# Optimization experiments

Measured on AMD Instinct MI355X. Metric: run time of the kernel, lower is better.

The kernel has to match this reference:

```python
import jax, jax.numpy as jnp
import numpy as np

B, T, HID = 4, 2048, 1024
NH = 16
HS = HID // NH  # 64


def setup_inputs() -> dict:
    key = jax.random.key(0)
    ks = jax.random.split(key, 9)
    s = 1.0 / np.sqrt(HID)
    return {
        "x": jax.random.normal(ks[0], (B, T, HID), dtype=jnp.float32),
        "Wq": jax.random.uniform(ks[1], (HID, HID), jnp.float32, -s, s),
        "bq": jax.random.uniform(ks[2], (HID,), jnp.float32, -s, s),
        "Wk": jax.random.uniform(ks[3], (HID, HID), jnp.float32, -s, s),
        "bk": jax.random.uniform(ks[4], (HID,), jnp.float32, -s, s),
        "Wv": jax.random.uniform(ks[5], (HID, HS), jnp.float32, -s, s),
        "bv": jax.random.uniform(ks[6], (HS,), jnp.float32, -s, s),
        "Wo": jax.random.uniform(ks[7], (HS, HID), jnp.float32, -1.0 / np.sqrt(HS), 1.0 / np.sqrt(HS)),
        "bo": jax.random.uniform(ks[8], (HID,), jnp.float32, -1.0 / np.sqrt(HS), 1.0 / np.sqrt(HS)),
    }


def reference(x, Wq, bq, Wk, bk, Wv, bv, Wo, bo):
    scale = HS ** -0.5
    q = (x @ Wq + bq).reshape(B, T, NH, HS)  # (B,T,H,hs)
    k = (x @ Wk + bk).reshape(B, T, NH, HS)
    v = x @ Wv + bv                          # shared V: (B,T,hs)
    # scores: (B,H,T,T)
    scores = jnp.einsum("bqhd,bkhd->bhqk", q, k) * scale
    attn = jax.nn.softmax(scores, axis=-1)
    attn_avg = attn.mean(axis=1)             # (B,T,T), head-averaged
    out = jnp.einsum("bqk,bkd->bqd", attn_avg, v) @ Wo + bo  # (B,T,HID)
    return out, attn_avg
```

## Files before the change

### kernel.cpp

```cpp
#include <hip/hip_runtime.h>
#include <math.h>

#define Bc   4
#define Tt   2048
#define HIDc 1024
#define NHc  16
#define HSc  64
#define BTc  (Bc * Tt)
#define QSCALE 0.18033688011112042f

typedef __attribute__((ext_vector_type(8))) short bf16x8;
typedef __attribute__((ext_vector_type(4))) float f32x4;

__device__ __forceinline__ unsigned short f2bf(float f) {
    unsigned u = __float_as_uint(f);
    u = u + 0x7FFFu + ((u >> 16) & 1u);
    return (unsigned short)(u >> 16);
}

__device__ __forceinline__ float fexp2(float x) {
#if __has_builtin(__builtin_amdgcn_exp2f)
    return __builtin_amdgcn_exp2f(x);
#else
    float r; asm("v_exp_f32 %0, %1" : "=v"(r) : "v"(x)); return r;
#endif
}

__global__ __launch_bounds__(256) void gemm_f32(
    const float* __restrict__ A, const float* __restrict__ Bm,
    const float* __restrict__ bias, float* __restrict__ C,
    int M, int N, int K, long sA, long sB, long sC)
{
    A  += (long)blockIdx.z * sA;
    Bm += (long)blockIdx.z * sB;
    C  += (long)blockIdx.z * sC;

    __shared__ float As[16][64];
    __shared__ float Bs[16][64];

    const int tid  = threadIdx.x;
    const int tx   = tid & 15;
    const int ty   = tid >> 4;
    const int row0 = blockIdx.y * 64;
    const int col0 = blockIdx.x * 64;

    const int la_r = tid >> 2;
    const int la_c = (tid & 3) << 2;
    const int lb_r = tid >> 4;
    const int lb_c = (tid & 15) << 2;

    float acc[4][4] = {};

    for (int k0 = 0; k0 < K; k0 += 16) {
        float4 av = *(const float4*)&A[(long)(row0 + la_r) * K + k0 + la_c];
        float4 bv = *(const float4*)&Bm[(long)(k0 + lb_r) * N + col0 + lb_c];
        __syncthreads();
        As[la_c + 0][la_r] = av.x;
        As[la_c + 1][la_r] = av.y;
        As[la_c + 2][la_r] = av.z;
        As[la_c + 3][la_r] = av.w;
        *(float4*)&Bs[lb_r][lb_c] = bv;
        __syncthreads();
#pragma unroll
        for (int kk = 0; kk < 16; ++kk) {
            float4 a = *(float4*)&As[kk][ty << 2];
            float4 b = *(float4*)&Bs[kk][tx << 2];
            float ar[4] = {a.x, a.y, a.z, a.w};
            float br[4] = {b.x, b.y, b.z, b.w};
#pragma unroll
            for (int i = 0; i < 4; ++i)
#pragma unroll
                for (int j = 0; j < 4; ++j)
                    acc[i][j] = fmaf(ar[i], br[j], acc[i][j]);
        }
    }

    float4 bvv = make_float4(0.f, 0.f, 0.f, 0.f);
    if (bias) bvv = *(const float4*)&bias[col0 + (tx << 2)];
#pragma unroll
    for (int i = 0; i < 4; ++i) {
        int m = row0 + (ty << 2) + i;
        float4 o;
        o.x = acc[i][0] + bvv.x;
        o.y = acc[i][1] + bvv.y;
        o.z = acc[i][2] + bvv.z;
        o.w = acc[i][3] + bvv.w;
        *(float4*)&C[(long)m * N + col0 + (tx << 2)] = o;
    }
}

__global__ __launch_bounds__(256) void init_bias64(
    float* __restrict__ C, const float* __restrict__ bias, long n)
{
    long idx = (long)blockIdx.x * 256 + threadIdx.x;
    if (idx < n) C[idx] = bias ? bias[idx & 63] : 0.f;
}

__global__ __launch_bounds__(256) void cast_bf16(
    const float* __restrict__ src, unsigned short* __restrict__ dst, long n)
{
    long i = ((long)blockIdx.x * 256 + threadIdx.x) * 4;
    if (i >= n) return;
    float4 v = *(const float4*)&src[i];
    ushort4 o;
    o.x = f2bf(v.x); o.y = f2bf(v.y); o.z = f2bf(v.z); o.w = f2bf(v.w);
    *(ushort4*)&dst[i] = o;
}

__global__ __launch_bounds__(256) void transpose_cast(
    const float* __restrict__ W, unsigned short* __restrict__ Wt, int R, int C)
{
    __shared__ float t[32][33];
    const int k0 = blockIdx.x * 32, n0 = blockIdx.y * 32;
    const int c = threadIdx.x & 31, r = threadIdx.x >> 5;
#pragma unroll
    for (int rr = r; rr < 32; rr += 8)
        t[rr][c] = W[(long)(k0 + rr) * C + n0 + c];
    __syncthreads();
#pragma unroll
    for (int rr = r; rr < 32; rr += 8)
        Wt[(long)(n0 + rr) * R + k0 + c] = f2bf(t[c][rr]);
}

__global__ __launch_bounds__(256) void gemm_bt_bf16(
    const unsigned short* __restrict__ A, const unsigned short* __restrict__ Bt,
    const float* __restrict__ bias, unsigned short* __restrict__ C,
    int M, int N, int K, float oscale)
{
    __shared__ unsigned short As[128][72];
    __shared__ unsigned short Bs[128][72];

    const int tid  = threadIdx.x;
    const int row0 = blockIdx.y * 128;
    const int col0 = blockIdx.x * 128;
    const int w  = tid >> 6, L = tid & 63;
    const int wm = (w & 1) * 64, wn = (w >> 1) * 64;
    const int lr = tid >> 3;
    const int lc = (tid & 7) * 8;
    const int ml = L & 15, q8 = (L >> 4) * 8, q4 = (L >> 4) * 4;

    f32x4 acc[4][4];
#pragma unroll
    for (int i = 0; i < 4; ++i)
#pragma unroll
        for (int j = 0; j < 4; ++j)
            acc[i][j] = (f32x4){0.f, 0.f, 0.f, 0.f};

    for (int k0 = 0; k0 < K; k0 += 64) {
        __syncthreads();
#pragma unroll
        for (int rr = 0; rr < 128; rr += 32) {
            *(float4*)&As[lr + rr][lc] = *(const float4*)&A[(long)(row0 + lr + rr) * K + k0 + lc];
            *(float4*)&Bs[lr + rr][lc] = *(const float4*)&Bt[(long)(col0 + lr + rr) * K + k0 + lc];
        }
        __syncthreads();
#pragma unroll
        for (int kk = 0; kk < 64; kk += 32) {
            bf16x8 a[4], b[4];
#pragma unroll
            for (int i = 0; i < 4; ++i) a[i] = *(bf16x8*)&As[wm + i * 16 + ml][kk + q8];
#pragma unroll
            for (int j = 0; j < 4; ++j) b[j] = *(bf16x8*)&Bs[wn + j * 16 + ml][kk + q8];
#pragma unroll
            for (int i = 0; i < 4; ++i)
#pragma unroll
                for (int j = 0; j < 4; ++j)
                    acc[i][j] = __builtin_amdgcn_mfma_f32_16x16x32_bf16(a[i], b[j], acc[i][j], 0, 0, 0);
        }
    }

#pragma unroll
    for (int j = 0; j < 4; ++j) {
        const int col = col0 + wn + j * 16 + ml;
        const float bj = bias ? bias[col] : 0.f;
#pragma unroll
        for (int i = 0; i < 4; ++i) {
#pragma unroll
            for (int r = 0; r < 4; ++r) {
                const int row = row0 + wm + i * 16 + q4 + r;
                C[(long)row * N + col] = f2bf((acc[i][j][r] + bj) * oscale);
            }
        }
    }
}

__global__ __launch_bounds__(256) void gemm_v_bf16(
    const unsigned short* __restrict__ A, const unsigned short* __restrict__ Bt,
    float* __restrict__ C)
{
    __shared__ unsigned short As[128][72];
    __shared__ unsigned short Bs[64][72];

    const int tid  = threadIdx.x;
    const int row0 = blockIdx.x * 128;
    const int kbeg = blockIdx.y * 256;
    const int w = tid >> 6, L = tid & 63;
    const int ml = L & 15, q8 = (L >> 4) * 8, q4 = (L >> 4) * 4;
    const int ar = tid >> 3, ac = (tid & 7) * 8;
    const int br = tid >> 2, bc = (tid & 3) * 16;

    f32x4 acc[2][4];
#pragma unroll
    for (int i = 0; i < 2; ++i)
#pragma unroll
        for (int j = 0; j < 4; ++j) acc[i][j] = (f32x4){0.f, 0.f, 0.f, 0.f};

    for (int k0 = kbeg; k0 < kbeg + 256; k0 += 64) {
        __syncthreads();
#pragma unroll
        for (int rr = 0; rr < 128; rr += 32)
            *(float4*)&As[ar + rr][ac] = *(const float4*)&A[(long)(row0 + ar + rr) * HIDc + k0 + ac];
        *(float4*)&Bs[br][bc]     = *(const float4*)&Bt[(long)br * HIDc + k0 + bc];
        *(float4*)&Bs[br][bc + 8] = *(const float4*)&Bt[(long)br * HIDc + k0 + bc + 8];
        __syncthreads();
#pragma unroll
        for (int kk = 0; kk < 64; kk += 32) {
            bf16x8 a[2], b[4];
#pragma unroll
            for (int i = 0; i < 2; ++i) a[i] = *(bf16x8*)&As[w * 32 + i * 16 + ml][kk + q8];
#pragma unroll
            for (int j = 0; j < 4; ++j) b[j] = *(bf16x8*)&Bs[j * 16 + ml][kk + q8];
#pragma unroll
            for (int i = 0; i < 2; ++i)
#pragma unroll
                for (int j = 0; j < 4; ++j)
                    acc[i][j] = __builtin_amdgcn_mfma_f32_16x16x32_bf16(a[i], b[j], acc[i][j], 0, 0, 0);
        }
    }

#pragma unroll
    for (int i = 0; i < 2; ++i)
#pragma unroll
        for (int j = 0; j < 4; ++j)
#pragma unroll
            for (int r = 0; r < 4; ++r)
                atomicAdd(&C[(long)(row0 + w * 32 + i * 16 + q4 + r) * 64 + j * 16 + ml], acc[i][j][r]);
}

__global__ __launch_bounds__(256) void attn_denom(
    const unsigned short* __restrict__ qb, const unsigned short* __restrict__ kb,
    float* __restrict__ linv)
{
    const int qt = blockIdx.x, h = blockIdx.y, b = blockIdx.z;
    __shared__ unsigned short Qs[128][72];
    __shared__ unsigned short Ks[64][72];

    const int tid = threadIdx.x;
    const int w = tid >> 6, L = tid & 63;
    const int ml = L & 15, q8 = (L >> 4) * 8, q4 = (L >> 4) * 4;
    const int ar = tid >> 3, ac = (tid & 7) * 8;
    const int kr = tid >> 2, kc = (tid & 3) * 16;

#pragma unroll
    for (int rr = 0; rr < 128; rr += 32)
        *(float4*)&Qs[ar + rr][ac] =
            *(const float4*)&qb[(long)(b * Tt + qt * 128 + ar + rr) * HIDc + h * HSc + ac];

    float lacc[2][4] = {};

    for (int kt = 0; kt < Tt / 64; ++kt) {
        const unsigned short* s = kb + ((long)(b * Tt + kt * 64 + kr) * HIDc + h * HSc + kc);
        float4 v0 = *(const float4*)s;
        float4 v1 = *(const float4*)(s + 8);
        __syncthreads();
        *(float4*)&Ks[kr][kc]     = v0;
        *(float4*)&Ks[kr][kc + 8] = v1;
        __syncthreads();

        f32x4 acc[2][4];
#pragma unroll
        for (int i = 0; i < 2; ++i)
#pragma unroll
            for (int j = 0; j < 4; ++j) acc[i][j] = (f32x4){0.f, 0.f, 0.f, 0.f};
#pragma unroll
        for (int kk = 0; kk < 64; kk += 32) {
            bf16x8 a[2], bfr[4];
#pragma unroll
            for (int i = 0; i < 2; ++i) a[i] = *(bf16x8*)&Qs[w * 32 + i * 16 + ml][kk + q8];
#pragma unroll
            for (int j = 0; j < 4; ++j) bfr[j] = *(bf16x8*)&Ks[j * 16 + ml][kk + q8];
#pragma unroll
            for (int i = 0; i < 2; ++i)
#pragma unroll
                for (int j = 0; j < 4; ++j)
                    acc[i][j] = __builtin_amdgcn_mfma_f32_16x16x32_bf16(a[i], bfr[j], acc[i][j], 0, 0, 0);
        }
#pragma unroll
        for (int i = 0; i < 2; ++i)
#pragma unroll
            for (int j = 0; j < 4; ++j)
#pragma unroll
                for (int r = 0; r < 4; ++r)
                    lacc[i][r] += fexp2(acc[i][j][r]);
    }

#pragma unroll
    for (int i = 0; i < 2; ++i)
#pragma unroll
        for (int r = 0; r < 4; ++r) {
            float v = lacc[i][r];
            v += __shfl_xor(v, 1, 16);
            v += __shfl_xor(v, 2, 16);
            v += __shfl_xor(v, 4, 16);
            v += __shfl_xor(v, 8, 16);
            if (ml == 0)
                linv[((long)(b * NHc + h)) * Tt + qt * 128 + w * 32 + i * 16 + q4 + r] =
                    1.0f / (v * (float)NHc);
        }
}

__global__ __launch_bounds__(256) void attn_avg_w(
    const unsigned short* __restrict__ qb, const unsigned short* __restrict__ kb,
    const float* __restrict__ linv, const float* __restrict__ v,
    float* __restrict__ attn, float* __restrict__ o1)
{
    const int ktg = blockIdx.x, qt = blockIdx.y, b = blockIdx.z;

    __shared__ __align__(16) unsigned char smem[34816];
    unsigned short (*Qs)[72]   = (unsigned short(*)[72])smem;
    unsigned short (*Ks)[72]   = (unsigned short(*)[72])(smem + 9216);
    float* invs                = (float*)(smem + 27648);
    unsigned short (*Ps)[136]  = (unsigned short(*)[136])smem;
    unsigned short (*Vst)[136] = (unsigned short(*)[136])(smem + 17408);

    const int tid = threadIdx.x;
    const int w = tid >> 6, L = tid & 63;
    const int ml = L & 15, q8 = (L >> 4) * 8, q4 = (L >> 4) * 4;
    const int rw = (w >> 1) * 32;
    const int kh = (w & 1) * 64;
    const int qr = tid >> 2, qc = (tid & 3) * 16;
    const int kr = tid >> 3, kc = (tid & 7) * 8;

    float pacc[2][4][4] = {};

    for (int h = 0; h < NHc; ++h) {
        const unsigned short* sq = qb + ((long)(b * Tt + qt * 64 + qr) * HIDc + h * HSc + qc);
        float4 q0 = *(const float4*)sq;
        float4 q1 = *(const float4*)(sq + 8);
        float4 kv[4];
#pragma unroll
        for (int rr = 0; rr < 4; ++rr)
            kv[rr] = *(const float4*)&kb[(long)(b * Tt + ktg * 128 + kr + rr * 32) * HIDc + h * HSc + kc];
        float iv = 0.f;
        if (tid < 64) iv = linv[((long)(b * NHc + h)) * Tt + qt * 64 + tid];
        __syncthreads();
        *(float4*)&Qs[qr][qc]     = q0;
        *(float4*)&Qs[qr][qc + 8] = q1;
#pragma unroll
        for (int rr = 0; rr < 4; ++rr)
            *(float4*)&Ks[kr + rr * 32][kc] = kv[rr];
        if (tid < 64) invs[tid] = iv;
        __syncthreads();

        f32x4 acc[2][4];
#pragma unroll
        for (int i = 0; i < 2; ++i)
#pragma unroll
            for (int j = 0; j < 4; ++j) acc[i][j] = (f32x4){0.f, 0.f, 0.f, 0.f};
#pragma unroll
        for (int kk = 0; kk < 64; kk += 32) {
            bf16x8 a[2], bfr[4];
#pragma unroll
            for (int i = 0; i < 2; ++i) a[i] = *(bf16x8*)&Qs[rw + i * 16 + ml][kk + q8];
#pragma unroll
            for (int j = 0; j < 4; ++j) bfr[j] = *(bf16x8*)&Ks[kh + j * 16 + ml][kk + q8];
#pragma unroll
            for (int i = 0; i < 2; ++i)
#pragma unroll
                for (int j = 0; j < 4; ++j)
                    acc[i][j] = __builtin_amdgcn_mfma_f32_16x16x32_bf16(a[i], bfr[j], acc[i][j], 0, 0, 0);
        }
        float ivr[2][4];
#pragma unroll
        for (int i = 0; i < 2; ++i)
#pragma unroll
            for (int r = 0; r < 4; ++r) ivr[i][r] = invs[rw + i * 16 + q4 + r];
#pragma unroll
        for (int i = 0; i < 2; ++i)
#pragma unroll
            for (int j = 0; j < 4; ++j)
#pragma unroll
                for (int r = 0; r < 4; ++r)
                    pacc[i][j][r] += fexp2(acc[i][j][r]) * ivr[i][r];
    }

    __syncthreads();

#pragma unroll
    for (int i = 0; i < 2; ++i)
#pragma unroll
        for (int j = 0; j < 4; ++j)
#pragma unroll
            for (int r = 0; r < 4; ++r) {
                const int qrow = rw + i * 16 + q4 + r;
                const int col  = kh + j * 16 + ml;
                attn[((long)(b * Tt + qt * 64 + qrow)) * Tt + ktg * 128 + col] = pacc[i][j][r];
                Ps[qrow][col] = f2bf(pacc[i][j][r]);
            }
#pragma unroll
    for (int e = tid; e < 8192; e += 256) {
        const int r = e >> 6, d = e & 63;
        Vst[d][r] = f2bf(v[((long)(b * Tt + ktg * 128 + r)) * 64 + d]);
    }
    __syncthreads();

    const int qh = (w >> 1) * 32, dh = (w & 1) * 32;
    f32x4 uacc[2][2];
#pragma unroll
    for (int i = 0; i < 2; ++i)
#pragma unroll
        for (int j = 0; j < 2; ++j) uacc[i][j] = (f32x4){0.f, 0.f, 0.f, 0.f};
#pragma unroll
    for (int kk = 0; kk < 128; kk += 32) {
        bf16x8 a0 = *(bf16x8*)&Ps[qh + ml][kk + q8];
        bf16x8 a1 = *(bf16x8*)&Ps[qh + 16 + ml][kk + q8];
        bf16x8 b0 = *(bf16x8*)&Vst[dh + ml][kk + q8];
        bf16x8 b1 = *(bf16x8*)&Vst[dh + 16 + ml][kk + q8];
        uacc[0][0] = __builtin_amdgcn_mfma_f32_16x16x32_bf16(a0, b0, uacc[0][0], 0, 0, 0);
        uacc[0][1] = __builtin_amdgcn_mfma_f32_16x16x32_bf16(a0, b1, uacc[0][1], 0, 0, 0);
        uacc[1][0] = __builtin_amdgcn_mfma_f32_16x16x32_bf16(a1, b0, uacc[1][0], 0, 0, 0);
        uacc[1][1] = __builtin_amdgcn_mfma_f32_16x16x32_bf16(a1, b1, uacc[1][1], 0, 0, 0);
    }
#pragma unroll
    for (int i = 0; i < 2; ++i)
#pragma unroll
        for (int j = 0; j < 2; ++j)
#pragma unroll
            for (int r = 0; r < 4; ++r)
                atomicAdd(&o1[((long)(b * Tt + qt * 64 + qh + i * 16 + q4 + r)) * 64 + dh + j * 16 + ml],
                          uacc[i][j][r]);
}

extern "C" void kernel_launch(void* const* d_in, const int* in_sizes, int n_in,
                              void* d_out, int out_size, void* d_ws, size_t ws_size,
                              hipStream_t stream)
{
    const float* x  = (const float*)d_in[0];
    const float* Wq = (const float*)d_in[1];
    const float* bq = (const float*)d_in[2];
    const float* Wk = (const float*)d_in[3];
    const float* bk = (const float*)d_in[4];
    const float* Wv = (const float*)d_in[5];
    const float* bv = (const float*)d_in[6];
    const float* Wo = (const float*)d_in[7];
    const float* bo = (const float*)d_in[8];

    float* out  = (float*)d_out;
    float* attn = out + (long)BTc * HIDc;

    unsigned short* xb  = (unsigned short*)d_ws;
    unsigned short* Wqt = xb  + (long)BTc * HIDc;
    unsigned short* Wkt = Wqt + (long)HIDc * HIDc;
    unsigned short* Wvt = Wkt + (long)HIDc * HIDc;
    unsigned short* qb  = Wvt + (long)HSc * HIDc;
    unsigned short* kb  = qb  + (long)BTc * HIDc;
    float* v    = (float*)(kb + (long)BTc * HIDc);
    float* linv = v    + (long)BTc * HSc;
    float* o1   = linv + (long)Bc * NHc * Tt;

    dim3 blk(256);

    cast_bf16<<<dim3((BTc * HIDc) / 1024), blk, 0, stream>>>(x, xb, (long)BTc * HIDc);
    transpose_cast<<<dim3(32, 32), blk, 0, stream>>>(Wq, Wqt, HIDc, HIDc);
    transpose_cast<<<dim3(32, 32), blk, 0, stream>>>(Wk, Wkt, HIDc, HIDc);
    transpose_cast<<<dim3(32, 2),  blk, 0, stream>>>(Wv, Wvt, HIDc, HSc);
    init_bias64<<<dim3((BTc * HSc) / 256), blk, 0, stream>>>(v,  bv,      (long)BTc * HSc);
    init_bias64<<<dim3((BTc * HSc) / 256), blk, 0, stream>>>(o1, nullptr, (long)BTc * HSc);

    gemm_bt_bf16<<<dim3(HIDc / 128, BTc / 128), blk, 0, stream>>>(xb, Wqt, bq, qb, BTc, HIDc, HIDc, QSCALE);
    gemm_bt_bf16<<<dim3(HIDc / 128, BTc / 128), blk, 0, stream>>>(xb, Wkt, bk, kb, BTc, HIDc, HIDc, 1.0f);

    gemm_v_bf16<<<dim3(BTc / 128, HIDc / 256), blk, 0, stream>>>(xb, Wvt, v);

    attn_denom<<<dim3(Tt / 128, NHc, Bc), blk, 0, stream>>>(qb, kb, linv);

    attn_avg_w<<<dim3(Tt / 128, Tt / 64, Bc), blk, 0, stream>>>(qb, kb, linv, v, attn, o1);

    gemm_f32<<<dim3(HIDc / 64, BTc / 64, 1), blk, 0, stream>>>(o1, Wo, bo, out, BTc, HIDc, HSc, 0, 0, 0);
}
```

Measured before the change: 446.3 us.

## Split PV product into separate GEMM, prefetch Q/K tiles, drop atomics

Removes the fused P·V step and its atomicAdds from attn_avg_w. The head-averaged attention is instead written to the output and read back by a new gemm_pv kernel, which splits the key dimension in half into two partial buffers that are summed when gemm_f32 loads its A operand. V is transposed and cast to bf16 up front by reusing the weight workspaces. attn_denom and attn_avg_w now register-prefetch the next K/Q tile during the current one, and all per-head inverse denominators are loaded into shared memory once. The cost is re-reading the large fp32 attention matrix from memory, in exchange for avoiding atomic contention and gaining better overlap.

```diff
diff --git a/kernel.cpp b/kernel.cpp
--- a/kernel.cpp
+++ b/kernel.cpp
@@ -27,14 +27,10 @@
 }
 
 __global__ __launch_bounds__(256) void gemm_f32(
-    const float* __restrict__ A, const float* __restrict__ Bm,
-    const float* __restrict__ bias, float* __restrict__ C,
-    int M, int N, int K, long sA, long sB, long sC)
-{
-    A  += (long)blockIdx.z * sA;
-    Bm += (long)blockIdx.z * sB;
-    C  += (long)blockIdx.z * sC;
-
+    const float* __restrict__ A, const float* __restrict__ A2,
+    const float* __restrict__ Bm, const float* __restrict__ bias,
+    float* __restrict__ C, int M, int N, int K)
+{
     __shared__ float As[16][64];
     __shared__ float Bs[16][64];
 
@@ -53,6 +49,10 @@
 
     for (int k0 = 0; k0 < K; k0 += 16) {
         float4 av = *(const float4*)&A[(long)(row0 + la_r) * K + k0 + la_c];
+        if (A2) {
+            float4 a2 = *(const float4*)&A2[(long)(row0 + la_r) * K + k0 + la_c];
+            av.x += a2.x; av.y += a2.y; av.z += a2.z; av.w += a2.w;
+        }
         float4 bv = *(const float4*)&Bm[(long)(k0 + lb_r) * N + col0 + lb_c];
         __syncthreads();
         As[la_c + 0][la_r] = av.x;
@@ -256,15 +256,20 @@
         *(float4*)&Qs[ar + rr][ac] =
             *(const float4*)&qb[(long)(b * Tt + qt * 128 + ar + rr) * HIDc + h * HSc + ac];
 
+    const unsigned short* kbase = kb + ((long)(b * Tt + kr) * HIDc + h * HSc + kc);
+    float4 v0 = *(const float4*)kbase;
+    float4 v1 = *(const float4*)(kbase + 8);
+
     float lacc[2][4] = {};
 
     for (int kt = 0; kt < Tt / 64; ++kt) {
-        const unsigned short* s = kb + ((long)(b * Tt + kt * 64 + kr) * HIDc + h * HSc + kc);
-        float4 v0 = *(const float4*)s;
-        float4 v1 = *(const float4*)(s + 8);
-        __syncthreads();
         *(float4*)&Ks[kr][kc]     = v0;
         *(float4*)&Ks[kr][kc + 8] = v1;
+        if (kt + 1 < Tt / 64) {
+            const unsigned short* s = kbase + (long)(kt + 1) * 64 * HIDc;
+            v0 = *(const float4*)s;
+            v1 = *(const float4*)(s + 8);
+        }
         __syncthreads();
 
         f32x4 acc[2][4];
@@ -292,6 +297,7 @@
 #pragma unroll
                 for (int r = 0; r < 4; ++r)
                     lacc[i][r] += fexp2(acc[i][j][r]);
+        __syncthreads();
     }
 
 #pragma unroll
@@ -311,17 +317,13 @@
 
 __global__ __launch_bounds__(256) void attn_avg_w(
     const unsigned short* __restrict__ qb, const unsigned short* __restrict__ kb,
-    const float* __restrict__ linv, const float* __restrict__ v,
-    float* __restrict__ attn, float* __restrict__ o1)
+    const float* __restrict__ linv, float* __restrict__ attn)
 {
     const int ktg = blockIdx.x, qt = blockIdx.y, b = blockIdx.z;
 
-    __shared__ __align__(16) unsigned char smem[34816];
-    unsigned short (*Qs)[72]   = (unsigned short(*)[72])smem;
-    unsigned short (*Ks)[72]   = (unsigned short(*)[72])(smem + 9216);
-    float* invs                = (float*)(smem + 27648);
-    unsigned short (*Ps)[136]  = (unsigned short(*)[136])smem;
-    unsigned short (*Vst)[136] = (unsigned short(*)[136])(smem + 17408);
+    __shared__ unsigned short Qs[64][72];
+    __shared__ unsigned short Ks[128][72];
+    __shared__ float invsAll[NHc][64];
 
     const int tid = threadIdx.x;
     const int w = tid >> 6, L = tid & 63;
@@ -331,25 +333,39 @@
     const int qr = tid >> 2, qc = (tid & 3) * 16;
     const int kr = tid >> 3, kc = (tid & 7) * 8;
 
+    {
+        const int hh = tid >> 4, r4 = (tid & 15) * 4;
+        *(float4*)&invsAll[hh][r4] =
+            *(const float4*)&linv[((long)(b * NHc + hh)) * Tt + qt * 64 + r4];
+    }
+
+    const unsigned short* qbase = qb + ((long)(b * Tt + qt * 64 + qr) * HIDc + qc);
+    const unsigned short* kbase = kb + ((long)(b * Tt + ktg * 128 + kr) * HIDc + kc);
+
+    float4 q0 = *(const float4*)qbase;
+    float4 q1 = *(const float4*)(qbase + 8);
+    float4 kv[4];
+#pragma unroll
+    for (int rr = 0; rr < 4; ++rr)
+        kv[rr] = *(const float4*)(kbase + (long)rr * 32 * HIDc);
+
     float pacc[2][4][4] = {};
 
     for (int h = 0; h < NHc; ++h) {
-        const unsigned short* sq = qb + ((long)(b * Tt + qt * 64 + qr) * HIDc + h * HSc + qc);
-        float4 q0 = *(const float4*)sq;
-        float4 q1 = *(const float4*)(sq + 8);
-        float4 kv[4];
-#pragma unroll
-        for (int rr = 0; rr < 4; ++rr)
-            kv[rr] = *(const float4*)&kb[(long)(b * Tt + ktg * 128 + kr + rr * 32) * HIDc + h * HSc + kc];
-        float iv = 0.f;
-        if (tid < 64) iv = linv[((long)(b * NHc + h)) * Tt + qt * 64 + tid];
-        __syncthreads();
         *(float4*)&Qs[qr][qc]     = q0;
         *(float4*)&Qs[qr][qc + 8] = q1;
 #pragma unroll
         for (int rr = 0; rr < 4; ++rr)
             *(float4*)&Ks[kr + rr * 32][kc] = kv[rr];
-        if (tid < 64) invs[tid] = iv;
+        if (h + 1 < NHc) {
+            const unsigned short* sq = qbase + (h + 1) * HSc;
+            q0 = *(const float4*)sq;
+            q1 = *(const float4*)(sq + 8);
+            const unsigned short* sk = kbase + (h + 1) * HSc;
+#pragma unroll
+            for (int rr = 0; rr < 4; ++rr)
+                kv[rr] = *(const float4*)(sk + (long)rr * 32 * HIDc);
+        }
         __syncthreads();
 
         f32x4 acc[2][4];
@@ -371,10 +387,8 @@
                     acc[i][j] = __builtin_amdgcn_mfma_f32_16x16x32_bf16(a[i], bfr[j], acc[i][j], 0, 0, 0);
         }
         float ivr[2][4];
-#pragma unroll
-        for (int i = 0; i < 2; ++i)
-#pragma unroll
-            for (int r = 0; r < 4; ++r) ivr[i][r] = invs[rw + i * 16 + q4 + r];
+        *(float4*)&ivr[0][0] = *(const float4*)&invsAll[h][rw + q4];
+        *(float4*)&ivr[1][0] = *(const float4*)&invsAll[h][rw + 16 + q4];
 #pragma unroll
         for (int i = 0; i < 2; ++i)
 #pragma unroll
@@ -382,9 +396,8 @@
 #pragma unroll
                 for (int r = 0; r < 4; ++r)
                     pacc[i][j][r] += fexp2(acc[i][j][r]) * ivr[i][r];
-    }
-
-    __syncthreads();
+        __syncthreads();
+    }
 
 #pragma unroll
     for (int i = 0; i < 2; ++i)
@@ -395,40 +408,84 @@
                 const int qrow = rw + i * 16 + q4 + r;
                 const int col  = kh + j * 16 + ml;
                 attn[((long)(b * Tt + qt * 64 + qrow)) * Tt + ktg * 128 + col] = pacc[i][j][r];
-                Ps[qrow][col] = f2bf(pacc[i][j][r]);
             }
-#pragma unroll
-    for (int e = tid; e < 8192; e += 256) {
-        const int r = e >> 6, d = e & 63;
-        Vst[d][r] = f2bf(v[((long)(b * Tt + ktg * 128 + r)) * 64 + d]);
-    }
-    __syncthreads();
-
-    const int qh = (w >> 1) * 32, dh = (w & 1) * 32;
-    f32x4 uacc[2][2];
+}
+
+__global__ __launch_bounds__(256) void gemm_pv(
+    const float* __restrict__ attn, const unsigned short* __restrict__ vT,
+    float* __restrict__ o1a, float* __restrict__ o1b)
+{
+    const int qt = blockIdx.x, khalf = blockIdx.y, b = blockIdx.z;
+    float* o1p = khalf ? o1b : o1a;
+
+    __shared__ unsigned short Ps[64][72];
+    __shared__ unsigned short Vs[64][72];
+
+    const int tid = threadIdx.x;
+    const int w = tid >> 6, L = tid & 63;
+    const int ml = L & 15, q8 = (L >> 4) * 8, q4 = (L >> 4) * 4;
+    const int wq = (w >> 1) * 32, wd = (w & 1) * 32;
+    const int pr = tid >> 2, pc = (tid & 3) * 16;
+    const int vr = tid >> 3, vc = (tid & 7) * 8;
+
+    const float* abase = attn + ((long)(b * Tt + qt * 64 + pr)) * Tt + khalf * 1024 + pc;
+    const unsigned short* vbase = vT + ((long)(b * HSc + vr)) * Tt + khalf * 1024 + vc;
+
+    float4 pf[4], vf0, vf1;
+#pragma unroll
+    for (int i = 0; i < 4; ++i) pf[i] = *(const float4*)(abase + i * 4);
+    vf0 = *(const float4*)vbase;
+    vf1 = *(const float4*)(vbase + (long)32 * Tt);
+
+    f32x4 acc[2][2];
 #pragma unroll
     for (int i = 0; i < 2; ++i)
 #pragma unroll
-        for (int j = 0; j < 2; ++j) uacc[i][j] = (f32x4){0.f, 0.f, 0.f, 0.f};
-#pragma unroll
-    for (int kk = 0; kk < 128; kk += 32) {
-        bf16x8 a0 = *(bf16x8*)&Ps[qh + ml][kk + q8];
-        bf16x8 a1 = *(bf16x8*)&Ps[qh + 16 + ml][kk + q8];
-        bf16x8 b0 = *(bf16x8*)&Vst[dh + ml][kk + q8];
-        bf16x8 b1 = *(bf16x8*)&Vst[dh + 16 + ml][kk + q8];
-        uacc[0][0] = __builtin_amdgcn_mfma_f32_16x16x32_bf16(a0, b0, uacc[0][0], 0, 0, 0);
-        uacc[0][1] = __builtin_amdgcn_mfma_f32_16x16x32_bf16(a0, b1, uacc[0][1], 0, 0, 0);
-        uacc[1][0] = __builtin_amdgcn_mfma_f32_16x16x32_bf16(a1, b0, uacc[1][0], 0, 0, 0);
-        uacc[1][1] = __builtin_amdgcn_mfma_f32_16x16x32_bf16(a1, b1, uacc[1][1], 0, 0, 0);
-    }
+        for (int j = 0; j < 2; ++j) acc[i][j] = (f32x4){0.f, 0.f, 0.f, 0.f};
+
+    for (int t = 0; t < 16; ++t) {
+        __align__(16) unsigned short tmp[16];
+#pragma unroll
+        for (int i = 0; i < 4; ++i) {
+            tmp[i * 4 + 0] = f2bf(pf[i].x);
+            tmp[i * 4 + 1] = f2bf(pf[i].y);
+            tmp[i * 4 + 2] = f2bf(pf[i].z);
+            tmp[i * 4 + 3] = f2bf(pf[i].w);
+        }
+        *(float4*)&Ps[pr][pc]      = *(float4*)&tmp[0];
+        *(float4*)&Ps[pr][pc + 8]  = *(float4*)&tmp[8];
+        *(float4*)&Vs[vr][vc]      = vf0;
+        *(float4*)&Vs[vr + 32][vc] = vf1;
+        if (t + 1 < 16) {
+#pragma unroll
+            for (int i = 0; i < 4; ++i)
+                pf[i] = *(const float4*)(abase + (t + 1) * 64 + i * 4);
+            vf0 = *(const float4*)(vbase + (t + 1) * 64);
+            vf1 = *(const float4*)(vbase + (long)32 * Tt + (t + 1) * 64);
+        }
+        __syncthreads();
+#pragma unroll
+        for (int kk = 0; kk < 64; kk += 32) {
+            bf16x8 a0 = *(bf16x8*)&Ps[wq + ml][kk + q8];
+            bf16x8 a1 = *(bf16x8*)&Ps[wq + 16 + ml][kk + q8];
+            bf16x8 b0 = *(bf16x8*)&Vs[wd + ml][kk + q8];
+            bf16x8 b1 = *(bf16x8*)&Vs[wd + 16 + ml][kk + q8];
+            acc[0][0] = __builtin_amdgcn_mfma_f32_16x16x32_bf16(a0, b0, acc[0][0], 0, 0, 0);
+            acc[0][1] = __builtin_amdgcn_mfma_f32_16x16x32_bf16(a0, b1, acc[0][1], 0, 0, 0);
+            acc[1][0] = __builtin_amdgcn_mfma_f32_16x16x32_bf16(a1, b0, acc[1][0], 0, 0, 0);
+            acc[1][1] = __builtin_amdgcn_mfma_f32_16x16x32_bf16(a1, b1, acc[1][1], 0, 0, 0);
+        }
+        __syncthreads();
+    }
+
 #pragma unroll
     for (int i = 0; i < 2; ++i)
 #pragma unroll
         for (int j = 0; j < 2; ++j)
 #pragma unroll
             for (int r = 0; r < 4; ++r)
-                atomicAdd(&o1[((long)(b * Tt + qt * 64 + qh + i * 16 + q4 + r)) * 64 + dh + j * 16 + ml],
-                          uacc[i][j][r]);
+                o1p[((long)(b * Tt + qt * 64 + wq + i * 16 + q4 + r)) * HSc + wd + j * 16 + ml] =
+                    acc[i][j][r];
 }
 
 extern "C" void kernel_launch(void* const* d_in, const int* in_sizes, int n_in,
@@ -456,7 +513,9 @@
     unsigned short* kb  = qb  + (long)BTc * HIDc;
     float* v    = (float*)(kb + (long)BTc * HIDc);
     float* linv = v    + (long)BTc * HSc;
-    float* o1   = linv + (long)Bc * NHc * Tt;
+    float* o1a  = linv + (long)Bc * NHc * Tt;
+    unsigned short* vbT = Wqt;
+    float* o1b = (float*)Wkt;
 
     dim3 blk(256);
 
@@ -464,17 +523,22 @@
     transpose_cast<<<dim3(32, 32), blk, 0, stream>>>(Wq, Wqt, HIDc, HIDc);
     transpose_cast<<<dim3(32, 32), blk, 0, stream>>>(Wk, Wkt, HIDc, HIDc);
     transpose_cast<<<dim3(32, 2),  blk, 0, stream>>>(Wv, Wvt, HIDc, HSc);
-    init_bias64<<<dim3((BTc * HSc) / 256), blk, 0, stream>>>(v,  bv,      (long)BTc * HSc);
-    init_bias64<<<dim3((BTc * HSc) / 256), blk, 0, stream>>>(o1, nullptr, (long)BTc * HSc);
+    init_bias64<<<dim3((BTc * HSc) / 256), blk, 0, stream>>>(v, bv, (long)BTc * HSc);
 
     gemm_bt_bf16<<<dim3(HIDc / 128, BTc / 128), blk, 0, stream>>>(xb, Wqt, bq, qb, BTc, HIDc, HIDc, QSCALE);
     gemm_bt_bf16<<<dim3(HIDc / 128, BTc / 128), blk, 0, stream>>>(xb, Wkt, bk, kb, BTc, HIDc, HIDc, 1.0f);
 
     gemm_v_bf16<<<dim3(BTc / 128, HIDc / 256), blk, 0, stream>>>(xb, Wvt, v);
 
+    for (int bi = 0; bi < Bc; ++bi)
+        transpose_cast<<<dim3(Tt / 32, HSc / 32), blk, 0, stream>>>(
+            v + (long)bi * Tt * HSc, vbT + (long)bi * HSc * Tt, Tt, HSc);
+
     attn_denom<<<dim3(Tt / 128, NHc, Bc), blk, 0, stream>>>(qb, kb, linv);
 
-    attn_avg_w<<<dim3(Tt / 128, Tt / 64, Bc), blk, 0, stream>>>(qb, kb, linv, v, attn, o1);
-
-    gemm_f32<<<dim3(HIDc / 64, BTc / 64, 1), blk, 0, stream>>>(o1, Wo, bo, out, BTc, HIDc, HSc, 0, 0, 0);
-}
+    attn_avg_w<<<dim3(Tt / 128, Tt / 64, Bc), blk, 0, stream>>>(qb, kb, linv, attn);
+
+    gemm_pv<<<dim3(Tt / 64, 2, Bc), blk, 0, stream>>>(attn, vbT, o1a, o1b);
+
+    gemm_f32<<<dim3(HIDc / 64, BTc / 64), blk, 0, stream>>>(o1a, o1b, Wo, bo, out, BTc, HIDc, HSc);
+}
```

Result: slower. 466.6 us (+4.6%).

## Remap blocks for XCD locality, enlarge attention tile, prefetch Q/K tiles

Applied to the files above, without the earlier changes.

Blocks of the GEMMs, denominator and attention-average kernels are now launched on a 1D grid and remapped so that consecutive blocks on the same XCD share rows and batches, which aims to improve L2 reuse on MI355X's chiplets. The attention-average kernel grows its query tile from 64 to 128 rows per block, halving the grid and the redundant K loads per query. It also preloads all head inverse-denominators into shared memory and register-prefetches the next head's Q/K. The denominator kernel gets the same register prefetch. The cost is more registers and shared memory per block (52 KB), which can reduce occupancy.

```diff
diff --git a/kernel.cpp b/kernel.cpp
--- a/kernel.cpp
+++ b/kernel.cpp
@@ -29,12 +29,8 @@
 __global__ __launch_bounds__(256) void gemm_f32(
     const float* __restrict__ A, const float* __restrict__ Bm,
     const float* __restrict__ bias, float* __restrict__ C,
-    int M, int N, int K, long sA, long sB, long sC)
-{
-    A  += (long)blockIdx.z * sA;
-    Bm += (long)blockIdx.z * sB;
-    C  += (long)blockIdx.z * sC;
-
+    int M, int N, int K)
+{
     __shared__ float As[16][64];
     __shared__ float Bs[16][64];
 
@@ -130,9 +126,12 @@
     __shared__ unsigned short As[128][72];
     __shared__ unsigned short Bs[128][72];
 
+    const int gid = blockIdx.x;
+    const int xcd = gid & 7, ii = gid >> 3;
+    const int row0 = (xcd * 8 + (ii >> 3)) * 128;
+    const int col0 = (ii & 7) * 128;
+
     const int tid  = threadIdx.x;
-    const int row0 = blockIdx.y * 128;
-    const int col0 = blockIdx.x * 128;
     const int w  = tid >> 6, L = tid & 63;
     const int wm = (w & 1) * 64, wn = (w >> 1) * 64;
     const int lr = tid >> 3;
@@ -191,9 +190,12 @@
     __shared__ unsigned short As[128][72];
     __shared__ unsigned short Bs[64][72];
 
+    const int gid = blockIdx.x;
+    const int xcd = gid & 7, ii = gid >> 3;
+    const int row0 = (xcd * 8 + (ii >> 2)) * 128;
+    const int kbeg = (ii & 3) * 256;
+
     const int tid  = threadIdx.x;
-    const int row0 = blockIdx.x * 128;
-    const int kbeg = blockIdx.y * 256;
     const int w = tid >> 6, L = tid & 63;
     const int ml = L & 15, q8 = (L >> 4) * 8, q4 = (L >> 4) * 4;
     const int ar = tid >> 3, ac = (tid & 7) * 8;
@@ -241,7 +243,12 @@
     const unsigned short* __restrict__ qb, const unsigned short* __restrict__ kb,
     float* __restrict__ linv)
 {
-    const int qt = blockIdx.x, h = blockIdx.y, b = blockIdx.z;
+    const int gid = blockIdx.x;
+    const int xcd = gid & 7, ii = gid >> 3;
+    const int bh  = xcd * 8 + (ii >> 4);
+    const int qt  = ii & 15;
+    const int b   = bh >> 4, h = bh & 15;
+
     __shared__ unsigned short Qs[128][72];
     __shared__ unsigned short Ks[64][72];
 
@@ -256,15 +263,20 @@
         *(float4*)&Qs[ar + rr][ac] =
             *(const float4*)&qb[(long)(b * Tt + qt * 128 + ar + rr) * HIDc + h * HSc + ac];
 
+    const unsigned short* kbase = kb + ((long)(b * Tt + kr) * HIDc + h * HSc + kc);
+    float4 v0 = *(const float4*)kbase;
+    float4 v1 = *(const float4*)(kbase + 8);
+
     float lacc[2][4] = {};
 
     for (int kt = 0; kt < Tt / 64; ++kt) {
-        const unsigned short* s = kb + ((long)(b * Tt + kt * 64 + kr) * HIDc + h * HSc + kc);
-        float4 v0 = *(const float4*)s;
-        float4 v1 = *(const float4*)(s + 8);
-        __syncthreads();
         *(float4*)&Ks[kr][kc]     = v0;
         *(float4*)&Ks[kr][kc + 8] = v1;
+        if (kt + 1 < Tt / 64) {
+            const unsigned short* s = kbase + (long)(kt + 1) * 64 * HIDc;
+            v0 = *(const float4*)s;
+            v1 = *(const float4*)(s + 8);
+        }
         __syncthreads();
 
         f32x4 acc[2][4];
@@ -292,6 +304,7 @@
 #pragma unroll
                 for (int r = 0; r < 4; ++r)
                     lacc[i][r] += fexp2(acc[i][j][r]);
+        __syncthreads();
     }
 
 #pragma unroll
@@ -314,87 +327,105 @@
     const float* __restrict__ linv, const float* __restrict__ v,
     float* __restrict__ attn, float* __restrict__ o1)
 {
-    const int ktg = blockIdx.x, qt = blockIdx.y, b = blockIdx.z;
-
-    __shared__ __align__(16) unsigned char smem[34816];
+    const int gid = blockIdx.x;
+    const int xcd = gid & 7, ii = gid >> 3;
+    const int b = xcd >> 1, qhalf = xcd & 1;
+    const int t = ii >> 4, u = ii & 15;
+    const int qt  = qhalf * 8 + (t & 1) * 4 + (u >> 2);
+    const int ktg = (t >> 1) * 4 + (u & 3);
+
+    __shared__ __align__(16) unsigned char smem[52224];
     unsigned short (*Qs)[72]   = (unsigned short(*)[72])smem;
-    unsigned short (*Ks)[72]   = (unsigned short(*)[72])(smem + 9216);
-    float* invs                = (float*)(smem + 27648);
+    unsigned short (*Ks)[72]   = (unsigned short(*)[72])(smem + 18432);
+    float (*invsAll)[128]      = (float(*)[128])(smem + 36864);
     unsigned short (*Ps)[136]  = (unsigned short(*)[136])smem;
-    unsigned short (*Vst)[136] = (unsigned short(*)[136])(smem + 17408);
+    unsigned short (*Vst)[136] = (unsigned short(*)[136])(smem + 34816);
 
     const int tid = threadIdx.x;
     const int w = tid >> 6, L = tid & 63;
     const int ml = L & 15, q8 = (L >> 4) * 8, q4 = (L >> 4) * 4;
-    const int rw = (w >> 1) * 32;
-    const int kh = (w & 1) * 64;
-    const int qr = tid >> 2, qc = (tid & 3) * 16;
-    const int kr = tid >> 3, kc = (tid & 7) * 8;
-
-    float pacc[2][4][4] = {};
+    const int wq = (w >> 1) * 64;
+    const int wk = (w & 1) * 64;
+    const int sr = tid >> 1, sc = (tid & 1) * 32;
+
+    {
+        const int hh = tid >> 4, r8 = (tid & 15) * 8;
+        *(float4*)&invsAll[hh][r8]     =
+            *(const float4*)&linv[((long)(b * NHc + hh)) * Tt + qt * 128 + r8];
+        *(float4*)&invsAll[hh][r8 + 4] =
+            *(const float4*)&linv[((long)(b * NHc + hh)) * Tt + qt * 128 + r8 + 4];
+    }
+
+    const unsigned short* qbase = qb + ((long)(b * Tt + qt * 128 + sr) * HIDc + sc);
+    const unsigned short* kbase = kb + ((long)(b * Tt + ktg * 128 + sr) * HIDc + sc);
+
+    float4 qv[4], kv[4];
+#pragma unroll
+    for (int c = 0; c < 4; ++c) {
+        qv[c] = *(const float4*)(qbase + c * 8);
+        kv[c] = *(const float4*)(kbase + c * 8);
+    }
+
+    float pacc[4][4][4] = {};
 
     for (int h = 0; h < NHc; ++h) {
-        const unsigned short* sq = qb + ((long)(b * Tt + qt * 64 + qr) * HIDc + h * HSc + qc);
-        float4 q0 = *(const float4*)sq;
-        float4 q1 = *(const float4*)(sq + 8);
-        float4 kv[4];
-#pragma unroll
-        for (int rr = 0; rr < 4; ++rr)
-            kv[rr] = *(const float4*)&kb[(long)(b * Tt + ktg * 128 + kr + rr * 32) * HIDc + h * HSc + kc];
-        float iv = 0.f;
-        if (tid < 64) iv = linv[((long)(b * NHc + h)) * Tt + qt * 64 + tid];
-        __syncthreads();
-        *(float4*)&Qs[qr][qc]     = q0;
-        *(float4*)&Qs[qr][qc + 8] = q1;
-#pragma unroll
-        for (int rr = 0; rr < 4; ++rr)
-            *(float4*)&Ks[kr + rr * 32][kc] = kv[rr];
-        if (tid < 64) invs[tid] = iv;
-        __syncthreads();
-
-        f32x4 acc[2][4];
-#pragma unroll
-        for (int i = 0; i < 2; ++i)
+#pragma unroll
+        for (int c = 0; c < 4; ++c) {
+            *(float4*)&Qs[sr][sc + c * 8] = qv[c];
+            *(float4*)&Ks[sr][sc + c * 8] = kv[c];
+        }
+        if (h + 1 < NHc) {
+            const unsigned short* sq = qbase + (h + 1) * HSc;
+            const unsigned short* sk = kbase + (h + 1) * HSc;
+#pragma unroll
+            for (int c = 0; c < 4; ++c) {
+                qv[c] = *(const float4*)(sq + c * 8);
+                kv[c] = *(const float4*)(sk + c * 8);
+            }
+        }
+        __syncthreads();
+
+        f32x4 acc[4][4];
+#pragma unroll
+        for (int i = 0; i < 4; ++i)
 #pragma unroll
             for (int j = 0; j < 4; ++j) acc[i][j] = (f32x4){0.f, 0.f, 0.f, 0.f};
 #pragma unroll
         for (int kk = 0; kk < 64; kk += 32) {
-            bf16x8 a[2], bfr[4];
-#pragma unroll
-            for (int i = 0; i < 2; ++i) a[i] = *(bf16x8*)&Qs[rw + i * 16 + ml][kk + q8];
-#pragma unroll
-            for (int j = 0; j < 4; ++j) bfr[j] = *(bf16x8*)&Ks[kh + j * 16 + ml][kk + q8];
-#pragma unroll
-            for (int i = 0; i < 2; ++i)
+            bf16x8 a[4], bfr[4];
+#pragma unroll
+            for (int i = 0; i < 4; ++i) a[i]   = *(bf16x8*)&Qs[wq + i * 16 + ml][kk + q8];
+#pragma unroll
+            for (int j = 0; j < 4; ++j) bfr[j] = *(bf16x8*)&Ks[wk + j * 16 + ml][kk + q8];
+#pragma unroll
+            for (int i = 0; i < 4; ++i)
 #pragma unroll
                 for (int j = 0; j < 4; ++j)
                     acc[i][j] = __builtin_amdgcn_mfma_f32_16x16x32_bf16(a[i], bfr[j], acc[i][j], 0, 0, 0);
         }
-        float ivr[2][4];
-#pragma unroll
-        for (int i = 0; i < 2; ++i)
-#pragma unroll
-            for (int r = 0; r < 4; ++r) ivr[i][r] = invs[rw + i * 16 + q4 + r];
-#pragma unroll
-        for (int i = 0; i < 2; ++i)
+        float ivr[4][4];
+#pragma unroll
+        for (int i = 0; i < 4; ++i)
+            *(float4*)&ivr[i][0] = *(const float4*)&invsAll[h][wq + i * 16 + q4];
+#pragma unroll
+        for (int i = 0; i < 4; ++i)
 #pragma unroll
             for (int j = 0; j < 4; ++j)
 #pragma unroll
                 for (int r = 0; r < 4; ++r)
                     pacc[i][j][r] += fexp2(acc[i][j][r]) * ivr[i][r];
-    }
-
-    __syncthreads();
-
-#pragma unroll
-    for (int i = 0; i < 2; ++i)
+        __syncthreads();
+    }
+
+#pragma unroll
+    for (int i = 0; i < 4; ++i)
 #pragma unroll
         for (int j = 0; j < 4; ++j)
 #pragma unroll
             for (int r = 0; r < 4; ++r) {
-                const int qrow = rw + i * 16 + q4 + r;
-                const int col  = kh + j * 16 + ml;
-                attn[((long)(b * Tt + qt * 64 + qrow)) * Tt + ktg * 128 + col] = pacc[i][j][r];
+                const int qrow = wq + i * 16 + q4 + r;
+                const int col  = wk + j * 16 + ml;
+                attn[((long)(b * Tt + qt * 128 + qrow)) * Tt + ktg * 128 + col] = pacc[i][j][r];
                 Ps[qrow][col] = f2bf(pacc[i][j][r]);
             }
 #pragma unroll
@@ -404,30 +435,32 @@
     }
     __syncthreads();
 
-    const int qh = (w >> 1) * 32, dh = (w & 1) * 32;
-    f32x4 uacc[2][2];
-#pragma unroll
-    for (int i = 0; i < 2; ++i)
+    const int wd = (w & 1) * 32;
+    f32x4 uacc[4][2];
+#pragma unroll
+    for (int i = 0; i < 4; ++i)
 #pragma unroll
         for (int j = 0; j < 2; ++j) uacc[i][j] = (f32x4){0.f, 0.f, 0.f, 0.f};
 #pragma unroll
     for (int kk = 0; kk < 128; kk += 32) {
-        bf16x8 a0 = *(bf16x8*)&Ps[qh + ml][kk + q8];
-        bf16x8 a1 = *(bf16x8*)&Ps[qh + 16 + ml][kk + q8];
-        bf16x8 b0 = *(bf16x8*)&Vst[dh + ml][kk + q8];
-        bf16x8 b1 = *(bf16x8*)&Vst[dh + 16 + ml][kk + q8];
-        uacc[0][0] = __builtin_amdgcn_mfma_f32_16x16x32_bf16(a0, b0, uacc[0][0], 0, 0, 0);
-        uacc[0][1] = __builtin_amdgcn_mfma_f32_16x16x32_bf16(a0, b1, uacc[0][1], 0, 0, 0);
-        uacc[1][0] = __builtin_amdgcn_mfma_f32_16x16x32_bf16(a1, b0, uacc[1][0], 0, 0, 0);
-        uacc[1][1] = __builtin_amdgcn_mfma_f32_16x16x32_bf16(a1, b1, uacc[1][1], 0, 0, 0);
-    }
-#pragma unroll
-    for (int i = 0; i < 2; ++i)
+        bf16x8 a[4], bvv[2];
+#pragma unroll
+        for (int i = 0; i < 4; ++i) a[i]   = *(bf16x8*)&Ps[wq + i * 16 + ml][kk + q8];
+#pragma unroll
+        for (int j = 0; j < 2; ++j) bvv[j] = *(bf16x8*)&Vst[wd + j * 16 + ml][kk + q8];
+#pragma unroll
+        for (int i = 0; i < 4; ++i)
+#pragma unroll
+            for (int j = 0; j < 2; ++j)
+                uacc[i][j] = __builtin_amdgcn_mfma_f32_16x16x32_bf16(a[i], bvv[j], uacc[i][j], 0, 0, 0);
+    }
+#pragma unroll
+    for (int i = 0; i < 4; ++i)
 #pragma unroll
         for (int j = 0; j < 2; ++j)
 #pragma unroll
             for (int r = 0; r < 4; ++r)
-                atomicAdd(&o1[((long)(b * Tt + qt * 64 + qh + i * 16 + q4 + r)) * 64 + dh + j * 16 + ml],
+                atomicAdd(&o1[((long)(b * Tt + qt * 128 + wq + i * 16 + q4 + r)) * 64 + wd + j * 16 + ml],
                           uacc[i][j][r]);
 }
 
@@ -467,14 +500,14 @@
     init_bias64<<<dim3((BTc * HSc) / 256), blk, 0, stream>>>(v,  bv,      (long)BTc * HSc);
     init_bias64<<<dim3((BTc * HSc) / 256), blk, 0, stream>>>(o1, nullptr, (long)BTc * HSc);
 
-    gemm_bt_bf16<<<dim3(HIDc / 128, BTc / 128), blk, 0, stream>>>(xb, Wqt, bq, qb, BTc, HIDc, HIDc, QSCALE);
-    gemm_bt_bf16<<<dim3(HIDc / 128, BTc / 128), blk, 0, stream>>>(xb, Wkt, bk, kb, BTc, HIDc, HIDc, 1.0f);
-
-    gemm_v_bf16<<<dim3(BTc / 128, HIDc / 256), blk, 0, stream>>>(xb, Wvt, v);
-
-    attn_denom<<<dim3(Tt / 128, NHc, Bc), blk, 0, stream>>>(qb, kb, linv);
-
-    attn_avg_w<<<dim3(Tt / 128, Tt / 64, Bc), blk, 0, stream>>>(qb, kb, linv, v, attn, o1);
-
-    gemm_f32<<<dim3(HIDc / 64, BTc / 64, 1), blk, 0, stream>>>(o1, Wo, bo, out, BTc, HIDc, HSc, 0, 0, 0);
-}
+    gemm_bt_bf16<<<dim3(512), blk, 0, stream>>>(xb, Wqt, bq, qb, BTc, HIDc, HIDc, QSCALE);
+    gemm_bt_bf16<<<dim3(512), blk, 0, stream>>>(xb, Wkt, bk, kb, BTc, HIDc, HIDc, 1.0f);
+
+    gemm_v_bf16<<<dim3(256), blk, 0, stream>>>(xb, Wvt, v);
+
+    attn_denom<<<dim3(1024), blk, 0, stream>>>(qb, kb, linv);
+
+    attn_avg_w<<<dim3(1024), blk, 0, stream>>>(qb, kb, linv, v, attn, o1);
+
+    gemm_f32<<<dim3(HIDc / 64, BTc / 64), blk, 0, stream>>>(o1, Wo, bo, out, BTc, HIDc, HSc);
+}
```

New measurement: 503.5 us. 12.8% more time.
